# Optimization experiments

Hardware: AMD Instinct MI355X
Metric: run time of the kernel (lower is better)

The kernel has to match this reference:

```python
import jax, jax.numpy as jnp
import numpy as np

DIM = 768
N_HEADS = 12
HEAD_DIM = DIM // N_HEADS
SCALE = HEAD_DIM ** (-0.5)


def setup_inputs() -> dict:
    key = jax.random.key(0)
    k1, k2, k3 = jax.random.split(key, 3)
    B, S = 8, 1024
    x = jax.random.normal(k1, (B, S, DIM), dtype=jnp.float32)
    qkv_w = jax.random.normal(k2, (3 * DIM, DIM), dtype=jnp.float32) * (DIM ** -0.5)
    qkv_b = jnp.zeros((3 * DIM,), dtype=jnp.float32)
    proj_w = jax.random.normal(k3, (DIM, DIM), dtype=jnp.float32) * (DIM ** -0.5)
    proj_b = jnp.zeros((DIM,), dtype=jnp.float32)
    return {"x": x, "qkv_w": qkv_w, "qkv_b": qkv_b, "proj_w": proj_w, "proj_b": proj_b}


def reference(x, qkv_w, qkv_b, proj_w, proj_b):
    B, S, D = x.shape
    # qkv projection: (B,S,3D)
    qkv = jnp.einsum('bsd,ed->bse', x, qkv_w) + qkv_b
    qkv = qkv.reshape(B, S, 3, N_HEADS, HEAD_DIM)
    q, k, v = qkv[:, :, 0], qkv[:, :, 1], qkv[:, :, 2]  # each (B,S,H,Dh)
    # scaled dot-product attention, materializing (B,H,S,S) as the original does
    scores = jnp.einsum('bqhd,bkhd->bhqk', q, k) * SCALE
    attn = jax.nn.softmax(scores, axis=-1)
    out = jnp.einsum('bhqk,bkhd->bqhd', attn, v).reshape(B, S, D)
    # output projection
    return jnp.einsum('bsd,ed->bse', out, proj_w) + proj_b
```

## Files before the change

### kernel.cpp

```cpp
#include <hip/hip_runtime.h>
#include <hip/hip_bf16.h>


typedef __attribute__((ext_vector_type(4)))  float f32x4;
typedef __attribute__((ext_vector_type(16))) float f32x16;
typedef __attribute__((ext_vector_type(8)))  short short8;
typedef __attribute__((ext_vector_type(4)))  short short4v;
typedef __attribute__((ext_vector_type(2)))  unsigned int uint2v;
typedef __attribute__((ext_vector_type(4)))  unsigned int uint4v;

__device__ __forceinline__ unsigned short f2bf_hw(float f) {
  return __builtin_bit_cast(unsigned short, __float2bfloat16(f));
}
__device__ __forceinline__ unsigned int pk2bf(float a, float b) {
  return (unsigned int)f2bf_hw(a) | ((unsigned int)f2bf_hw(b) << 16);
}

#define MFMA16(a, b, c) __builtin_amdgcn_mfma_f32_16x16x32_bf16((a), (b), (c), 0, 0, 0)
#define MFMA32(a, b, c) __builtin_amdgcn_mfma_f32_32x32x16_bf16((a), (b), (c), 0, 0, 0)

#define QSCALE 0.18033688011112042f

__device__ __forceinline__ void gload_lds16(const unsigned short* g, char* lds) {
  __builtin_amdgcn_global_load_lds(
      (const __attribute__((address_space(1))) unsigned int*)g,
      (__attribute__((address_space(3))) unsigned int*)lds, 16, 0, 0);
}

__global__ __launch_bounds__(256)
void cvt3(const float* __restrict__ a, unsigned short* __restrict__ da, int na,
          const float* __restrict__ b, unsigned short* __restrict__ db, int nb,
          const float* __restrict__ c, unsigned short* __restrict__ dc)
{
  int i = blockIdx.x * 256 + threadIdx.x;
  const float* s; unsigned short* d;
  if (i < na)           { s = a; d = da; }
  else if (i < na + nb) { s = b; d = db; i -= na; }
  else                  { s = c; d = dc; i -= na + nb; }
  f32x4 v = ((const f32x4*)s)[i];
  short4v h;
  h[0] = (short)f2bf_hw(v[0]); h[1] = (short)f2bf_hw(v[1]);
  h[2] = (short)f2bf_hw(v[2]); h[3] = (short)f2bf_hw(v[3]);
  ((short4v*)d)[i] = h;
}

template<int EPI>
__global__ __launch_bounds__(256)
void gemm_bt(const unsigned short* __restrict__ A, const unsigned short* __restrict__ Wb,
             const float* __restrict__ bias,
             unsigned short* __restrict__ Qt, unsigned short* __restrict__ Kt,
             unsigned short* __restrict__ Vt, float* __restrict__ Out)
{
  __shared__ char lds[65536];
  const int tid = threadIdx.x;
  const int w = tid >> 6, l = tid & 63, lr = l & 15, lg = l >> 4;
  const int wr = w >> 1, wc = w & 1;
  const int m0 = blockIdx.x * 128, n0 = blockIdx.y * 128;
  f32x4 acc[4][4] = {};

  const int srow = tid >> 3;
  const int cb   = ((tid & 7) << 4) ^ ((srow & 7) << 4);
  const unsigned short* pA = A  + (size_t)(m0 + srow) * 768 + (cb >> 1);
  const unsigned short* pW = Wb + (size_t)(n0 + srow) * 768 + (cb >> 1);
  char* const ldsA = lds + tid * 16;
  char* const ldsW = lds + 16384 + tid * 16;

  #pragma unroll
  for (int c = 0; c < 4; ++c) gload_lds16(pA + c * 32 * 768, ldsA + c * 4096);
  #pragma unroll
  for (int c = 0; c < 4; ++c) gload_lds16(pW + c * 32 * 768, ldsW + c * 4096);
  pA += 64; pW += 64;

  for (int kt = 0; kt < 12; ++kt) {
    if (kt < 11) {
      const int nb = ((kt + 1) & 1) * 32768;
      #pragma unroll
      for (int c = 0; c < 4; ++c) gload_lds16(pA + c * 32 * 768, ldsA + nb + c * 4096);
      #pragma unroll
      for (int c = 0; c < 4; ++c) gload_lds16(pW + c * 32 * 768, ldsW + nb + c * 4096);
      pA += 64; pW += 64;
      asm volatile("s_waitcnt vmcnt(8)" ::: "memory");
    } else {
      asm volatile("s_waitcnt vmcnt(0)" ::: "memory");
    }
    __builtin_amdgcn_s_barrier();
    __builtin_amdgcn_sched_barrier(0);

    const char* Ab = lds + (kt & 1) * 32768;
    const char* Bb = Ab + 16384;
    #pragma unroll
    for (int kc = 0; kc < 2; ++kc) {
      short8 af[4], bfr[4];
      #pragma unroll
      for (int mf = 0; mf < 4; ++mf) {
        const int row = wr * 64 + mf * 16 + lr;
        af[mf] = *(const short8*)(Ab + row * 128 +
                                  ((kc * 64 + lg * 16) ^ ((row & 7) << 4)));
      }
      #pragma unroll
      for (int nf = 0; nf < 4; ++nf) {
        const int row = wc * 64 + nf * 16 + lr;
        bfr[nf] = *(const short8*)(Bb + row * 128 +
                                   ((kc * 64 + lg * 16) ^ ((row & 7) << 4)));
      }
      #pragma unroll
      for (int mf = 0; mf < 4; ++mf)
        #pragma unroll
        for (int nf = 0; nf < 4; ++nf)
          acc[mf][nf] = MFMA16(af[mf], bfr[nf], acc[mf][nf]);
    }
    __builtin_amdgcn_s_barrier();
  }

  if constexpr (EPI == 0) {
    const int tt = blockIdx.y / 6;
    const int h = (blockIdx.y % 6) * 2 + wc;
    #pragma unroll
    for (int nf = 0; nf < 4; ++nf) {
      const int dh = nf * 16 + lr;
      const float bv = bias[n0 + wc * 64 + dh];
      #pragma unroll
      for (int mf = 0; mf < 4; ++mf) {
        const int mb = m0 + wr * 64 + mf * 16 + lg * 4;
        const int b_ = mb >> 10, s_ = mb & 1023;
        f32x4 c = acc[mf][nf];
        if (tt == 0) {
          unsigned short* p = Qt + ((b_ * 12 + h) * 1024 + s_) * 64 + dh;
          #pragma unroll
          for (int j = 0; j < 4; ++j) p[j * 64] = f2bf_hw((c[j] + bv) * QSCALE);
        } else if (tt == 1) {
          unsigned short* p = Kt + ((b_ * 12 + h) * 1024 + s_) * 64 + dh;
          #pragma unroll
          for (int j = 0; j < 4; ++j) p[j * 64] = f2bf_hw(c[j] + bv);
        } else {
          short4v pk;
          #pragma unroll
          for (int j = 0; j < 4; ++j) pk[j] = (short)f2bf_hw(c[j] + bv);
          *(short4v*)(Vt + ((b_ * 12 + h) * 64 + dh) * 1024 + s_) = pk;
        }
      }
    }
  } else {
    #pragma unroll
    for (int nf = 0; nf < 4; ++nf) {
      const int e = n0 + wc * 64 + nf * 16 + lr;
      const float bv = bias[e];
      #pragma unroll
      for (int mf = 0; mf < 4; ++mf) {
        const int mb = m0 + wr * 64 + mf * 16 + lg * 4;
        #pragma unroll
        for (int j = 0; j < 4; ++j)
          Out[(size_t)(mb + j) * 768 + e] = acc[mf][nf][j] + bv;
      }
    }
  }
}

__global__ __launch_bounds__(256, 3)
void attn_fwd(const unsigned short* __restrict__ Qt,
              const unsigned short* __restrict__ Kt,
              const unsigned short* __restrict__ Vt,
              unsigned short* __restrict__ AO)
{
  __shared__ char lds[49152];

  const int bid = blockIdx.x;
  const int bh = bid % 96, qt = bid / 96;
  const int tid = threadIdx.x, w = tid >> 6, l = tid & 63;
  const int l31 = l & 31, hi = l >> 5;
  const unsigned short* Qh = Qt + bh * 65536;
  const unsigned short* Kh = Kt + bh * 65536;
  const unsigned short* Vh = Vt + bh * 65536;
  const int b_ = bh / 12, h = bh % 12;

  const int srow = tid >> 3;
  const int cb   = ((tid & 7) << 4) ^ ((srow & 7) << 4);

  const int q0 = qt * 128 + w * 32;
  const unsigned short* qp = Qh + (size_t)(q0 + l31) * 64 + hi * 8;
  short8 bq[4];
  #pragma unroll
  for (int kk = 0; kk < 4; ++kk) bq[kk] = *(const short8*)(qp + kk * 16);

  #pragma unroll
  for (int c = 0; c < 2; ++c)
    gload_lds16(Kh + (size_t)(srow + c * 32) * 64 + (cb >> 1),
                lds + tid * 16 + c * 4096);
  #pragma unroll
  for (int c = 0; c < 2; ++c)
    gload_lds16(Vh + (size_t)(srow + c * 32) * 1024 + (cb >> 1),
                lds + 8192 + tid * 16 + c * 4096);

  float lsum = 0.f;
  f32x16 o0 = {}, o1 = {};

  const int kswz = (l31 & 7) << 4;
  const int vswz = kswz;

  int bc = 0, bn = 1;
  for (int t = 0; t < 16; ++t) {
    if (t < 15) {
      const int nk = (t + 1) * 64;
      char* const stK = lds + bn * 16384 + tid * 16;
      char* const stV = stK + 8192;
      #pragma unroll
      for (int c = 0; c < 2; ++c)
        gload_lds16(Kh + (size_t)(nk + srow + c * 32) * 64 + (cb >> 1),
                    stK + c * 4096);
      #pragma unroll
      for (int c = 0; c < 2; ++c)
        gload_lds16(Vh + (size_t)(srow + c * 32) * 1024 + nk + (cb >> 1),
                    stV + c * 4096);
      asm volatile("s_waitcnt vmcnt(4)" ::: "memory");
    } else {
      asm volatile("s_waitcnt vmcnt(0)" ::: "memory");
    }
    __builtin_amdgcn_s_barrier();
    __builtin_amdgcn_sched_barrier(0);

    const char* Kb = lds + bc * 16384;
    const char* Vb = Kb + 8192;
    const char* kbase0 = Kb + l31 * 128;
    const char* kbase1 = Kb + (32 + l31) * 128;

    f32x16 s0v = {}, s1v = {};
    __builtin_amdgcn_s_setprio(1);
    #pragma unroll
    for (int kk = 0; kk < 4; ++kk) {
      short8 ka = *(const short8*)(kbase0 + ((kk * 32 + hi * 16) ^ kswz));
      s0v = MFMA32(ka, bq[kk], s0v);
    }
    #pragma unroll
    for (int kk = 0; kk < 4; ++kk) {
      short8 ka = *(const short8*)(kbase1 + ((kk * 32 + hi * 16) ^ kswz));
      s1v = MFMA32(ka, bq[kk], s1v);
    }
    __builtin_amdgcn_s_setprio(0);

    #pragma unroll
    for (int kb = 0; kb < 2; ++kb) {
      const f32x16 s = kb ? s1v : s0v;

      unsigned int pk_[8];
      float t0 = 0.f, t1 = 0.f;
      #pragma unroll
      for (int i = 0; i < 8; ++i) {
        const float pa = __builtin_amdgcn_exp2f(s[2 * i]);
        const float pb = __builtin_amdgcn_exp2f(s[2 * i + 1]);
        if (i & 1) t1 += pa + pb; else t0 += pa + pb;
        pk_[i] = pk2bf(pa, pb);
      }
      lsum += t0 + t1;

      const uint2v r02 = __builtin_amdgcn_permlane32_swap(pk_[0], pk_[2], false, false);
      const uint2v r13 = __builtin_amdgcn_permlane32_swap(pk_[1], pk_[3], false, false);
      const uint2v r46 = __builtin_amdgcn_permlane32_swap(pk_[4], pk_[6], false, false);
      const uint2v r57 = __builtin_amdgcn_permlane32_swap(pk_[5], pk_[7], false, false);
      uint4v b0v, b1v;
      b0v[0] = r02[0]; b0v[1] = r13[0]; b0v[2] = r02[1]; b0v[3] = r13[1];
      b1v[0] = r46[0]; b1v[1] = r57[0]; b1v[2] = r46[1]; b1v[3] = r57[1];
      const short8 pb0 = __builtin_bit_cast(short8, b0v);
      const short8 pb1 = __builtin_bit_cast(short8, b1v);

      __builtin_amdgcn_s_setprio(1);
      #pragma unroll
      for (int kk = 0; kk < 2; ++kk) {
        const short8 pbk = kk ? pb1 : pb0;
        const int koff = kb * 64 + kk * 32 + hi * 16;
        short8 va0 = *(const short8*)(Vb + l31 * 128 + (koff ^ vswz));
        o0 = MFMA32(va0, pbk, o0);
        short8 va1 = *(const short8*)(Vb + (32 + l31) * 128 + (koff ^ vswz));
        o1 = MFMA32(va1, pbk, o1);
      }
      __builtin_amdgcn_s_setprio(0);
    }

    const int bt = bc; bc = bn; bn = 3 - bt - bn;
  }

  lsum += __shfl_xor(lsum, 32);
  const float inv = 1.f / lsum;
  unsigned short* aop = AO + ((size_t)(b_ * 1024 + q0 + l31)) * 768 + h * 64;
  #pragma unroll
  for (int g = 0; g < 4; ++g) {
    uint2v s0, s1;
    s0[0] = pk2bf(o0[4 * g] * inv,     o0[4 * g + 1] * inv);
    s0[1] = pk2bf(o0[4 * g + 2] * inv, o0[4 * g + 3] * inv);
    *(uint2v*)(aop + g * 8 + 4 * hi) = s0;
    s1[0] = pk2bf(o1[4 * g] * inv,     o1[4 * g + 1] * inv);
    s1[1] = pk2bf(o1[4 * g + 2] * inv, o1[4 * g + 3] * inv);
    *(uint2v*)(aop + 32 + g * 8 + 4 * hi) = s1;
  }
}

extern "C" void kernel_launch(void* const* d_in, const int* in_sizes, int n_in,
                              void* d_out, int out_size, void* d_ws, size_t ws_size,
                              hipStream_t stream)
{
  const float* x      = (const float*)d_in[0];
  const float* qkv_w  = (const float*)d_in[1];
  const float* qkv_b  = (const float*)d_in[2];
  const float* proj_w = (const float*)d_in[3];
  const float* proj_b = (const float*)d_in[4];
  float* out = (float*)d_out;

  unsigned short* ws = (unsigned short*)d_ws;
  unsigned short* xb  = ws;
  unsigned short* Qt  = ws + 6291456;
  unsigned short* Kt  = Qt + 6291456;
  unsigned short* Vt  = Kt + 6291456;
  unsigned short* qwb = Vt + 6291456;
  unsigned short* pwb = qwb + 1769472;
  unsigned short* AO  = xb;

  cvt3<<<8448, 256, 0, stream>>>(x, xb, 1572864, qkv_w, qwb, 442368, proj_w, pwb);
  gemm_bt<0><<<dim3(64, 18), 256, 0, stream>>>(xb, qwb, qkv_b, Qt, Kt, Vt, nullptr);
  attn_fwd<<<768, 256, 0, stream>>>(Qt, Kt, Vt, AO);
  gemm_bt<1><<<dim3(64, 6), 256, 0, stream>>>(AO, pwb, proj_b, nullptr, nullptr, nullptr, out);
}
```

Before: 103.0 us.

## Split attention key tiles across warp pairs and double the grid

Each attention block now covers 64 queries instead of 128. The four waves form two query slices times two key halves, and each wave processes 32 of the 64 keys per tile. Partial outputs and row sums from the second key half are reduced through LDS at the end. The buffer goes from triple to double buffering with 32KB of LDS, and the grid grows to 1536 blocks with a 5-block occupancy hint. The aim is more blocks and higher occupancy, at the cost of an extra barrier per iteration, reloading K/V once per 64 queries instead of once per 128, and a final LDS reduction.

```diff
diff --git a/kernel.cpp b/kernel.cpp
--- a/kernel.cpp
+++ b/kernel.cpp
@@ -156,18 +156,19 @@
   }
 }
 
-__global__ __launch_bounds__(256, 3)
+__global__ __launch_bounds__(256, 5)
 void attn_fwd(const unsigned short* __restrict__ Qt,
               const unsigned short* __restrict__ Kt,
               const unsigned short* __restrict__ Vt,
               unsigned short* __restrict__ AO)
 {
-  __shared__ char lds[49152];
+  __shared__ char lds[32768];
 
   const int bid = blockIdx.x;
   const int bh = bid % 96, qt = bid / 96;
   const int tid = threadIdx.x, w = tid >> 6, l = tid & 63;
   const int l31 = l & 31, hi = l >> 5;
+  const int kh = w >> 1, qs = w & 1;
   const unsigned short* Qh = Qt + bh * 65536;
   const unsigned short* Kh = Kt + bh * 65536;
   const unsigned short* Vh = Vt + bh * 65536;
@@ -176,7 +177,7 @@
   const int srow = tid >> 3;
   const int cb   = ((tid & 7) << 4) ^ ((srow & 7) << 4);
 
-  const int q0 = qt * 128 + w * 32;
+  const int q0 = qt * 64 + qs * 32;
   const unsigned short* qp = Qh + (size_t)(q0 + l31) * 64 + hi * 8;
   short8 bq[4];
   #pragma unroll
@@ -195,13 +196,12 @@
   f32x16 o0 = {}, o1 = {};
 
   const int kswz = (l31 & 7) << 4;
-  const int vswz = kswz;
-
-  int bc = 0, bn = 1;
+
   for (int t = 0; t < 16; ++t) {
+    const int cur = t & 1;
     if (t < 15) {
       const int nk = (t + 1) * 64;
-      char* const stK = lds + bn * 16384 + tid * 16;
+      char* const stK = lds + (cur ^ 1) * 16384 + tid * 16;
       char* const stV = stK + 8192;
       #pragma unroll
       for (int c = 0; c < 2; ++c)
@@ -218,78 +218,87 @@
     __builtin_amdgcn_s_barrier();
     __builtin_amdgcn_sched_barrier(0);
 
-    const char* Kb = lds + bc * 16384;
+    const char* Kb = lds + cur * 16384;
     const char* Vb = Kb + 8192;
-    const char* kbase0 = Kb + l31 * 128;
-    const char* kbase1 = Kb + (32 + l31) * 128;
-
-    f32x16 s0v = {}, s1v = {};
+    const char* kbase = Kb + (kh * 32 + l31) * 128;
+
+    f32x16 s = {};
     __builtin_amdgcn_s_setprio(1);
     #pragma unroll
     for (int kk = 0; kk < 4; ++kk) {
-      short8 ka = *(const short8*)(kbase0 + ((kk * 32 + hi * 16) ^ kswz));
-      s0v = MFMA32(ka, bq[kk], s0v);
-    }
-    #pragma unroll
-    for (int kk = 0; kk < 4; ++kk) {
-      short8 ka = *(const short8*)(kbase1 + ((kk * 32 + hi * 16) ^ kswz));
-      s1v = MFMA32(ka, bq[kk], s1v);
+      short8 ka = *(const short8*)(kbase + ((kk * 32 + hi * 16) ^ kswz));
+      s = MFMA32(ka, bq[kk], s);
     }
     __builtin_amdgcn_s_setprio(0);
 
-    #pragma unroll
-    for (int kb = 0; kb < 2; ++kb) {
-      const f32x16 s = kb ? s1v : s0v;
-
-      unsigned int pk_[8];
-      float t0 = 0.f, t1 = 0.f;
-      #pragma unroll
-      for (int i = 0; i < 8; ++i) {
-        const float pa = __builtin_amdgcn_exp2f(s[2 * i]);
-        const float pb = __builtin_amdgcn_exp2f(s[2 * i + 1]);
-        if (i & 1) t1 += pa + pb; else t0 += pa + pb;
-        pk_[i] = pk2bf(pa, pb);
-      }
-      lsum += t0 + t1;
-
-      const uint2v r02 = __builtin_amdgcn_permlane32_swap(pk_[0], pk_[2], false, false);
-      const uint2v r13 = __builtin_amdgcn_permlane32_swap(pk_[1], pk_[3], false, false);
-      const uint2v r46 = __builtin_amdgcn_permlane32_swap(pk_[4], pk_[6], false, false);
-      const uint2v r57 = __builtin_amdgcn_permlane32_swap(pk_[5], pk_[7], false, false);
-      uint4v b0v, b1v;
-      b0v[0] = r02[0]; b0v[1] = r13[0]; b0v[2] = r02[1]; b0v[3] = r13[1];
-      b1v[0] = r46[0]; b1v[1] = r57[0]; b1v[2] = r46[1]; b1v[3] = r57[1];
-      const short8 pb0 = __builtin_bit_cast(short8, b0v);
-      const short8 pb1 = __builtin_bit_cast(short8, b1v);
-
-      __builtin_amdgcn_s_setprio(1);
-      #pragma unroll
-      for (int kk = 0; kk < 2; ++kk) {
-        const short8 pbk = kk ? pb1 : pb0;
-        const int koff = kb * 64 + kk * 32 + hi * 16;
-        short8 va0 = *(const short8*)(Vb + l31 * 128 + (koff ^ vswz));
-        o0 = MFMA32(va0, pbk, o0);
-        short8 va1 = *(const short8*)(Vb + (32 + l31) * 128 + (koff ^ vswz));
-        o1 = MFMA32(va1, pbk, o1);
-      }
-      __builtin_amdgcn_s_setprio(0);
-    }
-
-    const int bt = bc; bc = bn; bn = 3 - bt - bn;
-  }
-
-  lsum += __shfl_xor(lsum, 32);
-  const float inv = 1.f / lsum;
-  unsigned short* aop = AO + ((size_t)(b_ * 1024 + q0 + l31)) * 768 + h * 64;
-  #pragma unroll
-  for (int g = 0; g < 4; ++g) {
-    uint2v s0, s1;
-    s0[0] = pk2bf(o0[4 * g] * inv,     o0[4 * g + 1] * inv);
-    s0[1] = pk2bf(o0[4 * g + 2] * inv, o0[4 * g + 3] * inv);
-    *(uint2v*)(aop + g * 8 + 4 * hi) = s0;
-    s1[0] = pk2bf(o1[4 * g] * inv,     o1[4 * g + 1] * inv);
-    s1[1] = pk2bf(o1[4 * g + 2] * inv, o1[4 * g + 3] * inv);
-    *(uint2v*)(aop + 32 + g * 8 + 4 * hi) = s1;
+    unsigned int pk_[8];
+    float t0 = 0.f, t1 = 0.f;
+    #pragma unroll
+    for (int i = 0; i < 8; ++i) {
+      const float pa = __builtin_amdgcn_exp2f(s[2 * i]);
+      const float pb = __builtin_amdgcn_exp2f(s[2 * i + 1]);
+      if (i & 1) t1 += pa + pb; else t0 += pa + pb;
+      pk_[i] = pk2bf(pa, pb);
+    }
+    lsum += t0 + t1;
+
+    const uint2v r02 = __builtin_amdgcn_permlane32_swap(pk_[0], pk_[2], false, false);
+    const uint2v r13 = __builtin_amdgcn_permlane32_swap(pk_[1], pk_[3], false, false);
+    const uint2v r46 = __builtin_amdgcn_permlane32_swap(pk_[4], pk_[6], false, false);
+    const uint2v r57 = __builtin_amdgcn_permlane32_swap(pk_[5], pk_[7], false, false);
+    uint4v b0v, b1v;
+    b0v[0] = r02[0]; b0v[1] = r13[0]; b0v[2] = r02[1]; b0v[3] = r13[1];
+    b1v[0] = r46[0]; b1v[1] = r57[0]; b1v[2] = r46[1]; b1v[3] = r57[1];
+    const short8 pb0 = __builtin_bit_cast(short8, b0v);
+    const short8 pb1 = __builtin_bit_cast(short8, b1v);
+
+    __builtin_amdgcn_s_setprio(1);
+    #pragma unroll
+    for (int kk = 0; kk < 2; ++kk) {
+      const short8 pbk = kk ? pb1 : pb0;
+      const int koff = kh * 64 + kk * 32 + hi * 16;
+      short8 va0 = *(const short8*)(Vb + l31 * 128 + (koff ^ kswz));
+      o0 = MFMA32(va0, pbk, o0);
+      short8 va1 = *(const short8*)(Vb + (32 + l31) * 128 + (koff ^ kswz));
+      o1 = MFMA32(va1, pbk, o1);
+    }
+    __builtin_amdgcn_s_setprio(0);
+
+    __builtin_amdgcn_s_barrier();
+  }
+
+  float* cm = (float*)lds;
+  if (kh == 1) {
+    float* p = cm + qs * (33 * 64);
+    #pragma unroll
+    for (int i = 0; i < 16; ++i) {
+      p[i * 64 + l] = o0[i];
+      p[(16 + i) * 64 + l] = o1[i];
+    }
+    p[32 * 64 + l] = lsum;
+  }
+  __builtin_amdgcn_s_barrier();
+  if (kh == 0) {
+    const float* p = cm + qs * (33 * 64);
+    #pragma unroll
+    for (int i = 0; i < 16; ++i) {
+      o0[i] += p[i * 64 + l];
+      o1[i] += p[(16 + i) * 64 + l];
+    }
+    lsum += p[32 * 64 + l];
+    lsum += __shfl_xor(lsum, 32);
+    const float inv = 1.f / lsum;
+    unsigned short* aop = AO + ((size_t)(b_ * 1024 + q0 + l31)) * 768 + h * 64;
+    #pragma unroll
+    for (int g = 0; g < 4; ++g) {
+      uint2v s0, s1;
+      s0[0] = pk2bf(o0[4 * g] * inv,     o0[4 * g + 1] * inv);
+      s0[1] = pk2bf(o0[4 * g + 2] * inv, o0[4 * g + 3] * inv);
+      *(uint2v*)(aop + g * 8 + 4 * hi) = s0;
+      s1[0] = pk2bf(o1[4 * g] * inv,     o1[4 * g + 1] * inv);
+      s1[1] = pk2bf(o1[4 * g + 2] * inv, o1[4 * g + 3] * inv);
+      *(uint2v*)(aop + 32 + g * 8 + 4 * hi) = s1;
+    }
   }
 }
 
@@ -315,6 +324,6 @@
 
   cvt3<<<8448, 256, 0, stream>>>(x, xb, 1572864, qkv_w, qwb, 442368, proj_w, pwb);
   gemm_bt<0><<<dim3(64, 18), 256, 0, stream>>>(xb, qwb, qkv_b, Qt, Kt, Vt, nullptr);
-  attn_fwd<<<768, 256, 0, stream>>>(Qt, Kt, Vt, AO);
+  attn_fwd<<<1536, 256, 0, stream>>>(Qt, Kt, Vt, AO);
   gemm_bt<1><<<dim3(64, 6), 256, 0, stream>>>(AO, pwb, proj_b, nullptr, nullptr, nullptr, out);
 }
```

After: 105.3 us. +2.2%, slower.
